# Optimization experiments

Measured on AMD Instinct MI355X. Metric: run time of the kernel, lower is better.

Reference implementation:

```python
import jax, jax.numpy as jnp
import numpy as np

N_NODES = 100000
N_EDGES = 1600000
D_IN = 128
D_HID = 128
N_CLS = 2


def gcn_conv(x, edge_index, W, b):
    """PyG GCNConv: add self-loops, symmetric normalization, linear, scatter-add, bias."""
    n = x.shape[0]
    loop = jnp.arange(n, dtype=edge_index.dtype)
    src = jnp.concatenate([edge_index[0], loop])  # [E+N]
    dst = jnp.concatenate([edge_index[1], loop])
    # degree computed on destination (col) after adding self-loops
    deg = jax.ops.segment_sum(jnp.ones_like(dst, dtype=x.dtype), dst, num_segments=n)
    dinv = jnp.where(deg > 0, jax.lax.rsqrt(deg), 0.0)
    norm = dinv[src] * dinv[dst]  # [E+N]
    h = x @ W  # [N, out]
    msg = h[src] * norm[:, None]  # [E+N, out]
    out = jax.ops.segment_sum(msg, dst, num_segments=n)
    return out + b


def setup_inputs() -> dict:
    key = jax.random.key(0)
    k1, k2, k3, k4 = jax.random.split(key, 4)
    x = jax.random.normal(k1, (N_NODES, D_IN), dtype=jnp.float32)
    edge_index = jax.random.randint(k2, (2, N_EDGES), 0, N_NODES, dtype=jnp.int64)
    W1 = jax.random.normal(k3, (D_IN, D_HID), dtype=jnp.float32) * (1.0 / np.sqrt(D_IN))
    b1 = jnp.zeros((D_HID,), dtype=jnp.float32)
    W2 = jax.random.normal(k4, (D_HID, N_CLS), dtype=jnp.float32) * (1.0 / np.sqrt(D_HID))
    b2 = jnp.zeros((N_CLS,), dtype=jnp.float32)
    return {"x": x, "edge_index": edge_index, "W1": W1, "b1": b1, "W2": W2, "b2": b2}


def reference(x, edge_index, W1, b1, W2, b2):
    h = gcn_conv(x, edge_index, W1, b1)
    h = jax.nn.relu(h)
    # training=False -> dropout skipped
    out = gcn_conv(h, edge_index, W2, b2)
    return out
```

## Files before the change

kernel.cpp:

```cpp
#include <hip/hip_runtime.h>
#include <hip/hip_fp16.h>
#include <cstdint>
#include <cstddef>

#define NN 100000
#define NE 1600000
#define D 128
#define NBK 782
#define NBLK_P 200
#define EPB 8000

typedef _Float16 half8 __attribute__((ext_vector_type(8)));
typedef _Float16 half4v __attribute__((ext_vector_type(4)));
typedef float f32x4 __attribute__((ext_vector_type(4)));


__launch_bounds__(256)
__global__ void p1_count_k(const int* __restrict__ ei, unsigned* __restrict__ offs) {
    __shared__ unsigned hist[NBK];
    int tid = threadIdx.x, b = blockIdx.x;
    for (int k = tid; k < NBK; k += 256) hist[k] = 0u;
    __syncthreads();
    int e0 = b * EPB;
    for (int i = tid; i < EPB; i += 256) {
        int d = ei[NE + e0 + i];
        atomicAdd(&hist[d >> 7], 1u);
    }
    __syncthreads();
    for (int k = tid; k < NBK; k += 256) offs[(size_t)b * NBK + k] = hist[k];
}

__launch_bounds__(256)
__global__ void p2a_k(unsigned* __restrict__ offs, unsigned* __restrict__ base) {
    __shared__ unsigned sh[256];
    int t = threadIdx.x, k = blockIdx.x;
    unsigned v = (t < NBLK_P) ? offs[(size_t)t * NBK + k] : 0u;
    sh[t] = v;
    __syncthreads();
    for (int off = 1; off < 256; off <<= 1) {
        unsigned u = (t >= off) ? sh[t - off] : 0u;
        __syncthreads();
        sh[t] += u;
        __syncthreads();
    }
    if (t < NBLK_P) offs[(size_t)t * NBK + k] = sh[t] - v;
    if (t == 255) base[k] = sh[255];
}

__global__ void p2b_k(unsigned* __restrict__ base) {
    __shared__ unsigned sh[1024];
    int t = threadIdx.x;
    unsigned v = (t < NBK) ? base[t] : 0u;
    sh[t] = v;
    __syncthreads();
    for (int off = 1; off < 1024; off <<= 1) {
        unsigned u = (t >= off) ? sh[t - off] : 0u;
        __syncthreads();
        sh[t] += u;
        __syncthreads();
    }
    if (t < NBK) base[t] = sh[t] - v;
    if (t == NBK) base[NBK] = sh[NBK - 1];
}

__launch_bounds__(256)
__global__ void p3_scatter_k(const int* __restrict__ ei, const unsigned* __restrict__ offs,
                             const unsigned* __restrict__ base, unsigned* __restrict__ part) {
    __shared__ unsigned lcnt[NBK];
    int tid = threadIdx.x, b = blockIdx.x;
    for (int k = tid; k < NBK; k += 256) lcnt[k] = base[k] + offs[(size_t)b * NBK + k];
    __syncthreads();
    int e0 = b * EPB;
    for (int i = tid; i < EPB; i += 256) {
        int s = ei[e0 + i];
        int d = ei[NE + e0 + i];
        unsigned pos = atomicAdd(&lcnt[d >> 7], 1u);
        part[pos] = (unsigned)s | ((unsigned)(d & 127) << 20);
    }
}

__launch_bounds__(256)
__global__ void p4_csr_k(const unsigned* __restrict__ part, const unsigned* __restrict__ base,
                         unsigned* __restrict__ rp, float* __restrict__ dinv,
                         unsigned* __restrict__ col) {
    __shared__ unsigned c[128], p[128], run[128];
    int tid = threadIdx.x, k = blockIdx.x;
    int n0 = k << 7;
    int nodes = (NN - n0 < 128) ? (NN - n0) : 128;
    unsigned e0 = base[k], e1 = base[k + 1];

    if (tid < 128) c[tid] = 0u;
    __syncthreads();
    for (unsigned e = e0 + tid; e < e1; e += 256)
        atomicAdd(&c[(part[e] >> 20) & 127], 1u);
    __syncthreads();

    unsigned myc = (tid < 128) ? c[tid] : 0u;
    if (tid < 128) p[tid] = myc;
    __syncthreads();
    for (int off = 1; off < 128; off <<= 1) {
        unsigned u = 0;
        if (tid < 128 && tid >= off) u = p[tid - off];
        __syncthreads();
        if (tid < 128) p[tid] += u;
        __syncthreads();
    }
    if (tid < 128) {
        unsigned excl = p[tid] - myc;
        run[tid] = excl;
        if (tid < nodes) {
            rp[n0 + tid] = e0 + excl;
            dinv[n0 + tid] = rsqrtf((float)(myc + 1u));
        }
    }
    if (k == 0 && tid == 0) rp[NN] = NE;
    __syncthreads();

    for (unsigned e = e0 + tid; e < e1; e += 256) {
        unsigned v = part[e];
        unsigned dlo = (v >> 20) & 127;
        unsigned pos = e0 + atomicAdd(&run[dlo], 1u);
        col[pos] = v & 0xFFFFFu;
    }
}

__global__ void wt_k(const float* __restrict__ W, _Float16* __restrict__ Wt) {
    int idx = blockIdx.x * 256 + threadIdx.x;
    int n = idx >> 7, k = idx & 127;
    Wt[idx] = (_Float16)W[k * 128 + n];
}

__launch_bounds__(256)
__global__ void gemm1_k(const float* __restrict__ x, const _Float16* __restrict__ Wt,
                        const float* __restrict__ dinv, _Float16* __restrict__ h) {
    __shared__ _Float16 wt[128 * 136];
    __shared__ _Float16 xs[64 * 136];
    int tid = threadIdx.x;
    int rb = blockIdx.x * 64;
    int w = tid >> 6, lane = tid & 63;
    int m = lane & 15, q4 = lane >> 4;

#pragma unroll
    for (int q = 0; q < 8; q++) {
        int idx = q * 256 + tid;
        int n  = idx >> 4;
        int k8 = (idx & 15) * 8;
        *(half8*)(&wt[n * 136 + k8]) = *(const half8*)(Wt + n * 128 + k8);
    }
#pragma unroll
    for (int q = 0; q < 8; q++) {
        int idx = q * 256 + tid;
        int row = idx >> 5;
        int c4 = (idx & 31) * 4;
        int gr = rb + row;
        float4 v = (gr < NN) ? *(const float4*)(x + (size_t)gr * 128 + c4)
                             : make_float4(0, 0, 0, 0);
        half4v hv = { (_Float16)v.x, (_Float16)v.y, (_Float16)v.z, (_Float16)v.w };
        *(half4v*)(&xs[row * 136 + c4]) = hv;
    }
    __syncthreads();

    f32x4 acc[8];
#pragma unroll
    for (int nt = 0; nt < 8; nt++) acc[nt] = (f32x4){0.f, 0.f, 0.f, 0.f};

    const _Float16* arow = &xs[(w * 16 + m) * 136 + q4 * 8];
#pragma unroll
    for (int kc = 0; kc < 4; kc++) {
        half8 af = *(const half8*)(arow + kc * 32);
#pragma unroll
        for (int nt = 0; nt < 8; nt++) {
            half8 bf = *(const half8*)(&wt[(nt * 16 + m) * 136 + q4 * 8 + kc * 32]);
            acc[nt] = __builtin_amdgcn_mfma_f32_16x16x32_f16(af, bf, acc[nt], 0, 0, 0);
        }
    }

    float dv[4];
#pragma unroll
    for (int r = 0; r < 4; r++) {
        int ri = rb + w * 16 + q4 * 4 + r;
        dv[r] = (ri < NN) ? dinv[ri] : 0.f;
    }
    __syncthreads();
#pragma unroll
    for (int nt = 0; nt < 8; nt++) {
#pragma unroll
        for (int r = 0; r < 4; r++) {
            xs[(w * 16 + q4 * 4 + r) * 136 + nt * 16 + m] = (_Float16)(acc[nt][r] * dv[r]);
        }
    }
    __syncthreads();
#pragma unroll
    for (int q = 0; q < 4; q++) {
        int idx = q * 256 + tid;
        int row = idx >> 4;
        int c8 = (idx & 15) * 8;
        int gr = rb + row;
        if (gr < NN)
            *(half8*)(h + (size_t)gr * 128 + c8) = *(const half8*)(&xs[row * 136 + c8]);
    }
}

#define GATHER(sv, vv) \
    { unsigned s_ = __builtin_amdgcn_readfirstlane(col[sv]); \
      vv = __half22float2(hb[(size_t)(s_ * 64u + lane)]); }

__launch_bounds__(256)
__global__ void agg1_k(const _Float16* __restrict__ h, const unsigned* __restrict__ rp,
                       const unsigned* __restrict__ col, const float* __restrict__ dinv,
                       const float* __restrict__ b1, const float* __restrict__ W2,
                       float* __restrict__ z) {
    int i = (blockIdx.x * 256 + threadIdx.x) >> 6;
    int lane = threadIdx.x & 63;
    if (i >= NN) return;

    const __half2* hb = (const __half2*)h;
    float di = dinv[i];
    float2 hv = __half22float2(hb[(size_t)i * 64 + lane]);
    float ax = hv.x, ay = hv.y;

    unsigned p0 = __builtin_amdgcn_readfirstlane(rp[i]);
    unsigned p1 = __builtin_amdgcn_readfirstlane(rp[i + 1]);
    unsigned e = p0;
    for (; e + 16 <= p1; e += 16) {
        float2 v0, v1, v2, v3, v4, v5, v6, v7, v8, v9, va, vb, vc, vd, ve, vf;
        GATHER(e, v0)      GATHER(e + 1, v1)  GATHER(e + 2, v2)  GATHER(e + 3, v3)
        GATHER(e + 4, v4)  GATHER(e + 5, v5)  GATHER(e + 6, v6)  GATHER(e + 7, v7)
        GATHER(e + 8, v8)  GATHER(e + 9, v9)  GATHER(e + 10, va) GATHER(e + 11, vb)
        GATHER(e + 12, vc) GATHER(e + 13, vd) GATHER(e + 14, ve) GATHER(e + 15, vf)
        ax += ((v0.x + v1.x) + (v2.x + v3.x)) + ((v4.x + v5.x) + (v6.x + v7.x))
            + ((v8.x + v9.x) + (va.x + vb.x)) + ((vc.x + vd.x) + (ve.x + vf.x));
        ay += ((v0.y + v1.y) + (v2.y + v3.y)) + ((v4.y + v5.y) + (v6.y + v7.y))
            + ((v8.y + v9.y) + (va.y + vb.y)) + ((vc.y + vd.y) + (ve.y + vf.y));
    }
    for (; e + 4 <= p1; e += 4) {
        float2 v0, v1, v2, v3;
        GATHER(e, v0) GATHER(e + 1, v1) GATHER(e + 2, v2) GATHER(e + 3, v3)
        ax += (v0.x + v1.x) + (v2.x + v3.x);
        ay += (v0.y + v1.y) + (v2.y + v3.y);
    }
    for (; e < p1; ++e) {
        float2 v;
        GATHER(e, v)
        ax += v.x;
        ay += v.y;
    }
    ax *= di;
    ay *= di;

    float2 bv = ((const float2*)b1)[lane];
    float h0 = fmaxf(ax + bv.x, 0.f);
    float h1 = fmaxf(ay + bv.y, 0.f);

    float4 w = ((const float4*)W2)[lane];
    float pz0 = fmaf(h0, w.x, h1 * w.z);
    float pz1 = fmaf(h0, w.y, h1 * w.w);
#pragma unroll
    for (int off = 32; off > 0; off >>= 1) {
        pz0 += __shfl_down(pz0, off);
        pz1 += __shfl_down(pz1, off);
    }
    if (lane == 0) {
        float2* zp = (float2*)(z + (size_t)i * 2);
        *zp = make_float2(pz0 * di, pz1 * di);
    }
}

__launch_bounds__(256)
__global__ void agg2_k(const float* __restrict__ z, const unsigned* __restrict__ rp,
                       const unsigned* __restrict__ col, const float* __restrict__ dinv,
                       const float* __restrict__ b2, float* __restrict__ out) {
    int i = (blockIdx.x * 256 + threadIdx.x) >> 4;
    int sl = threadIdx.x & 15;
    if (i >= NN) return;

    unsigned p0 = rp[i], p1 = rp[i + 1];
    float a0 = 0.f, a1 = 0.f;
    for (unsigned e = p0 + sl; e < p1; e += 16) {
        unsigned s = col[e];
        float2 v = ((const float2*)z)[s];
        a0 += v.x;
        a1 += v.y;
    }
#pragma unroll
    for (int off = 8; off > 0; off >>= 1) {
        a0 += __shfl_down(a0, off, 16);
        a1 += __shfl_down(a1, off, 16);
    }
    if (sl == 0) {
        float di = dinv[i];
        float2 zi = ((const float2*)z)[i];
        out[(size_t)i * 2]     = (a0 + zi.x) * di + b2[0];
        out[(size_t)i * 2 + 1] = (a1 + zi.y) * di + b2[1];
    }
}

extern "C" void kernel_launch(void* const* d_in, const int* in_sizes, int n_in,
                              void* d_out, int out_size, void* d_ws, size_t ws_size,
                              hipStream_t stream) {
    const float* x  = (const float*)d_in[0];
    const int*   ei = (const int*)d_in[1];
    const float* W1 = (const float*)d_in[2];
    const float* b1 = (const float*)d_in[3];
    const float* W2 = (const float*)d_in[4];
    const float* b2 = (const float*)d_in[5];
    float* out = (float*)d_out;

    char* ws = (char*)d_ws;
    unsigned* part = (unsigned*)(ws);
    unsigned* offs = (unsigned*)(ws + 6400000);
    unsigned* base = (unsigned*)(ws + 7100000);
    _Float16* h    = (_Float16*)(ws);
    float*    z    = (float*)(ws + 25600000);
    float*    dinv = (float*)(ws + 26400000);
    unsigned* rp   = (unsigned*)(ws + 26800000);
    unsigned* col  = (unsigned*)(ws + 27200016);
    _Float16* Wt   = (_Float16*)(ws + 33600016);

    wt_k<<<64, 256, 0, stream>>>(W1, Wt);
    p1_count_k<<<NBLK_P, 256, 0, stream>>>(ei, offs);
    p2a_k<<<NBK, 256, 0, stream>>>(offs, base);
    p2b_k<<<1, 1024, 0, stream>>>(base);
    p3_scatter_k<<<NBLK_P, 256, 0, stream>>>(ei, offs, base, part);
    p4_csr_k<<<NBK, 256, 0, stream>>>(part, base, rp, dinv, col);

    gemm1_k<<<(NN + 63) / 64, 256, 0, stream>>>(x, Wt, dinv, h);
    agg1_k<<<(NN + 3) / 4, 256, 0, stream>>>(h, rp, col, dinv, b1, W2, z);
    agg2_k<<<(NN * 16 + 255) / 256, 256, 0, stream>>>(z, rp, col, dinv, b2, out);
}
```

Measured before the change: 228.4 us.

## Fuse W transpose into count kernel, vectorize edge loads, enlarge GEMM row tile

The weight transpose kernel is folded into the first histogram kernel, which removes one launch. The count and scatter passes now read edge indices as int4 vectors, so each thread handles four edges per iteration. The GEMM tile grows from 64 to 128 rows per block, with K split into two 64-wide stages so each B fragment feeds two MFMAs, and the output is staged in the weight buffer. This halves the grid and amortizes the per-block weight load, at the cost of more accumulator registers and an extra barrier.

```diff
diff --git a/kernel.cpp b/kernel.cpp
--- a/kernel.cpp
+++ b/kernel.cpp
@@ -16,18 +16,28 @@
 
 
 __launch_bounds__(256)
-__global__ void p1_count_k(const int* __restrict__ ei, unsigned* __restrict__ offs) {
+__global__ void p1_count_k(const int* __restrict__ ei, unsigned* __restrict__ offs,
+                           const float* __restrict__ W, _Float16* __restrict__ Wt) {
     __shared__ unsigned hist[NBK];
     int tid = threadIdx.x, b = blockIdx.x;
     for (int k = tid; k < NBK; k += 256) hist[k] = 0u;
     __syncthreads();
     int e0 = b * EPB;
-    for (int i = tid; i < EPB; i += 256) {
-        int d = ei[NE + e0 + i];
-        atomicAdd(&hist[d >> 7], 1u);
+    for (int i = tid * 4; i < EPB; i += 1024) {
+        int4 d4 = *(const int4*)(ei + NE + e0 + i);
+        atomicAdd(&hist[d4.x >> 7], 1u);
+        atomicAdd(&hist[d4.y >> 7], 1u);
+        atomicAdd(&hist[d4.z >> 7], 1u);
+        atomicAdd(&hist[d4.w >> 7], 1u);
     }
     __syncthreads();
     for (int k = tid; k < NBK; k += 256) offs[(size_t)b * NBK + k] = hist[k];
+
+    if (b < 64) {
+        int idx = b * 256 + tid;
+        int n = idx >> 7, k = idx & 127;
+        Wt[idx] = (_Float16)W[k * 128 + n];
+    }
 }
 
 __launch_bounds__(256)
@@ -71,11 +81,14 @@
     for (int k = tid; k < NBK; k += 256) lcnt[k] = base[k] + offs[(size_t)b * NBK + k];
     __syncthreads();
     int e0 = b * EPB;
-    for (int i = tid; i < EPB; i += 256) {
-        int s = ei[e0 + i];
-        int d = ei[NE + e0 + i];
-        unsigned pos = atomicAdd(&lcnt[d >> 7], 1u);
-        part[pos] = (unsigned)s | ((unsigned)(d & 127) << 20);
+    for (int i = tid * 4; i < EPB; i += 1024) {
+        int4 s4 = *(const int4*)(ei + e0 + i);
+        int4 d4 = *(const int4*)(ei + NE + e0 + i);
+        unsigned p;
+        p = atomicAdd(&lcnt[d4.x >> 7], 1u); part[p] = (unsigned)s4.x | ((unsigned)(d4.x & 127) << 20);
+        p = atomicAdd(&lcnt[d4.y >> 7], 1u); part[p] = (unsigned)s4.y | ((unsigned)(d4.y & 127) << 20);
+        p = atomicAdd(&lcnt[d4.z >> 7], 1u); part[p] = (unsigned)s4.z | ((unsigned)(d4.z & 127) << 20);
+        p = atomicAdd(&lcnt[d4.w >> 7], 1u); part[p] = (unsigned)s4.w | ((unsigned)(d4.w & 127) << 20);
     }
 }
 
@@ -124,80 +137,83 @@
     }
 }
 
-__global__ void wt_k(const float* __restrict__ W, _Float16* __restrict__ Wt) {
-    int idx = blockIdx.x * 256 + threadIdx.x;
-    int n = idx >> 7, k = idx & 127;
-    Wt[idx] = (_Float16)W[k * 128 + n];
-}
-
 __launch_bounds__(256)
 __global__ void gemm1_k(const float* __restrict__ x, const _Float16* __restrict__ Wt,
                         const float* __restrict__ dinv, _Float16* __restrict__ h) {
     __shared__ _Float16 wt[128 * 136];
-    __shared__ _Float16 xs[64 * 136];
+    __shared__ _Float16 xs[128 * 72];
     int tid = threadIdx.x;
-    int rb = blockIdx.x * 64;
+    int rb = blockIdx.x * 128;
     int w = tid >> 6, lane = tid & 63;
     int m = lane & 15, q4 = lane >> 4;
 
 #pragma unroll
     for (int q = 0; q < 8; q++) {
         int idx = q * 256 + tid;
-        int n  = idx >> 4;
-        int k8 = (idx & 15) * 8;
+        int n = idx >> 4, k8 = (idx & 15) * 8;
         *(half8*)(&wt[n * 136 + k8]) = *(const half8*)(Wt + n * 128 + k8);
     }
+
+    f32x4 acc[2][8];
+#pragma unroll
+    for (int rt = 0; rt < 2; rt++)
+#pragma unroll
+        for (int nt = 0; nt < 8; nt++) acc[rt][nt] = (f32x4){0.f, 0.f, 0.f, 0.f};
+
+    for (int ks = 0; ks <= 64; ks += 64) {
+        if (ks) __syncthreads();
+#pragma unroll
+        for (int q = 0; q < 8; q++) {
+            int idx = q * 256 + tid;
+            int row = idx >> 4;
+            int c4 = (idx & 15) * 4;
+            int gr = rb + row;
+            float4 v = (gr < NN) ? *(const float4*)(x + (size_t)gr * 128 + ks + c4)
+                                 : make_float4(0, 0, 0, 0);
+            half4v hv = { (_Float16)v.x, (_Float16)v.y, (_Float16)v.z, (_Float16)v.w };
+            *(half4v*)(&xs[row * 72 + c4]) = hv;
+        }
+        __syncthreads();
+
+#pragma unroll
+        for (int kc = 0; kc < 2; kc++) {
+            half8 a0 = *(const half8*)(&xs[(w * 32 + m) * 72 + kc * 32 + q4 * 8]);
+            half8 a1 = *(const half8*)(&xs[(w * 32 + 16 + m) * 72 + kc * 32 + q4 * 8]);
+#pragma unroll
+            for (int nt = 0; nt < 8; nt++) {
+                half8 bf = *(const half8*)(&wt[(nt * 16 + m) * 136 + ks + kc * 32 + q4 * 8]);
+                acc[0][nt] = __builtin_amdgcn_mfma_f32_16x16x32_f16(a0, bf, acc[0][nt], 0, 0, 0);
+                acc[1][nt] = __builtin_amdgcn_mfma_f32_16x16x32_f16(a1, bf, acc[1][nt], 0, 0, 0);
+            }
+        }
+    }
+
+    float dv[2][4];
+#pragma unroll
+    for (int rt = 0; rt < 2; rt++)
+#pragma unroll
+        for (int r = 0; r < 4; r++) {
+            int ri = rb + w * 32 + rt * 16 + q4 * 4 + r;
+            dv[rt][r] = (ri < NN) ? dinv[ri] : 0.f;
+        }
+    __syncthreads();
+#pragma unroll
+    for (int rt = 0; rt < 2; rt++)
+#pragma unroll
+        for (int nt = 0; nt < 8; nt++)
+#pragma unroll
+            for (int r = 0; r < 4; r++)
+                wt[(w * 32 + rt * 16 + q4 * 4 + r) * 136 + nt * 16 + m] =
+                    (_Float16)(acc[rt][nt][r] * dv[rt][r]);
+    __syncthreads();
 #pragma unroll
     for (int q = 0; q < 8; q++) {
-        int idx = q * 256 + tid;
-        int row = idx >> 5;
-        int c4 = (idx & 31) * 4;
-        int gr = rb + row;
-        float4 v = (gr < NN) ? *(const float4*)(x + (size_t)gr * 128 + c4)
-                             : make_float4(0, 0, 0, 0);
-        half4v hv = { (_Float16)v.x, (_Float16)v.y, (_Float16)v.z, (_Float16)v.w };
-        *(half4v*)(&xs[row * 136 + c4]) = hv;
-    }
-    __syncthreads();
-
-    f32x4 acc[8];
-#pragma unroll
-    for (int nt = 0; nt < 8; nt++) acc[nt] = (f32x4){0.f, 0.f, 0.f, 0.f};
-
-    const _Float16* arow = &xs[(w * 16 + m) * 136 + q4 * 8];
-#pragma unroll
-    for (int kc = 0; kc < 4; kc++) {
-        half8 af = *(const half8*)(arow + kc * 32);
-#pragma unroll
-        for (int nt = 0; nt < 8; nt++) {
-            half8 bf = *(const half8*)(&wt[(nt * 16 + m) * 136 + q4 * 8 + kc * 32]);
-            acc[nt] = __builtin_amdgcn_mfma_f32_16x16x32_f16(af, bf, acc[nt], 0, 0, 0);
-        }
-    }
-
-    float dv[4];
-#pragma unroll
-    for (int r = 0; r < 4; r++) {
-        int ri = rb + w * 16 + q4 * 4 + r;
-        dv[r] = (ri < NN) ? dinv[ri] : 0.f;
-    }
-    __syncthreads();
-#pragma unroll
-    for (int nt = 0; nt < 8; nt++) {
-#pragma unroll
-        for (int r = 0; r < 4; r++) {
-            xs[(w * 16 + q4 * 4 + r) * 136 + nt * 16 + m] = (_Float16)(acc[nt][r] * dv[r]);
-        }
-    }
-    __syncthreads();
-#pragma unroll
-    for (int q = 0; q < 4; q++) {
         int idx = q * 256 + tid;
         int row = idx >> 4;
         int c8 = (idx & 15) * 8;
         int gr = rb + row;
         if (gr < NN)
-            *(half8*)(h + (size_t)gr * 128 + c8) = *(const half8*)(&xs[row * 136 + c8]);
+            *(half8*)(h + (size_t)gr * 128 + c8) = *(const half8*)(&wt[row * 136 + c8]);
     }
 }
 
@@ -317,14 +333,13 @@
     unsigned* col  = (unsigned*)(ws + 27200016);
     _Float16* Wt   = (_Float16*)(ws + 33600016);
 
-    wt_k<<<64, 256, 0, stream>>>(W1, Wt);
-    p1_count_k<<<NBLK_P, 256, 0, stream>>>(ei, offs);
+    p1_count_k<<<NBLK_P, 256, 0, stream>>>(ei, offs, W1, Wt);
     p2a_k<<<NBK, 256, 0, stream>>>(offs, base);
     p2b_k<<<1, 1024, 0, stream>>>(base);
     p3_scatter_k<<<NBLK_P, 256, 0, stream>>>(ei, offs, base, part);
     p4_csr_k<<<NBK, 256, 0, stream>>>(part, base, rp, dinv, col);
 
-    gemm1_k<<<(NN + 63) / 64, 256, 0, stream>>>(x, Wt, dinv, h);
+    gemm1_k<<<(NN + 127) / 128, 256, 0, stream>>>(x, Wt, dinv, h);
     agg1_k<<<(NN + 3) / 4, 256, 0, stream>>>(h, rp, col, dinv, b1, W2, z);
     agg2_k<<<(NN * 16 + 255) / 256, 256, 0, stream>>>(z, rp, col, dinv, b2, out);
 }
```

Result: faster. 223.9 us (-2.0%).
